# Performance work log

Hardware: AMD Instinct MI355X
Metric: run time of the kernel (lower is better)

The kernel has to match this reference:

```python
import jax, jax.numpy as jnp
import numpy as np
import math

B, C, H, W, K, HID = 8, 64, 512, 512, 8, 64

def setup_inputs() -> dict:
    key = jax.random.key(0)
    ks = jax.random.split(key, 12)
    s = 0.05  # weight scale
    return {
        "x": jax.random.normal(ks[0], (B, C, H, W), dtype=jnp.float32),
        "w1k": jax.random.normal(ks[1], (1, HID), dtype=jnp.float32) * s,
        "b1k": jax.random.normal(ks[2], (HID,), dtype=jnp.float32) * s,
        "w2k": jax.random.normal(ks[3], (HID, K * K), dtype=jnp.float32) * s,
        "b2k": jax.random.normal(ks[4], (K * K,), dtype=jnp.float32) * s,
        "w1b": jax.random.normal(ks[5], (1, HID), dtype=jnp.float32) * s,
        "b1b": jax.random.normal(ks[6], (HID,), dtype=jnp.float32) * s,
        "w2b": jax.random.normal(ks[7], (HID, 1), dtype=jnp.float32) * s,
        "b2b": jax.random.normal(ks[8], (1,), dtype=jnp.float32) * s,
        "conv_w": jax.random.normal(ks[9], (C, C), dtype=jnp.float32) * s,
        "conv_b": jax.random.normal(ks[10], (C,), dtype=jnp.float32) * s,
    }

def _patch_pos_dist(h, w, k):
    # normalized distance of each KxK patch center from the image center, row-major over (nh, nw)
    nh, nw = h // k, w // k
    cy, cx = h / 2.0, w / 2.0
    max_d = math.sqrt(cy ** 2 + cx ** 2)
    py = jnp.arange(nh, dtype=jnp.float32) * k + k / 2.0
    px = jnp.arange(nw, dtype=jnp.float32) * k + k / 2.0
    d = jnp.sqrt((py - cy)[:, None] ** 2 + (px - cx)[None, :] ** 2) / max_d
    return d.reshape(nh * nw)  # [L]

def reference(x, w1k, b1k, w2k, b2k, w1b, b1b, w2b, b2b, conv_w, conv_b):
    b, c, h, w = x.shape
    kk = w2k.shape[1]
    k = int(round(math.sqrt(kk)))
    nh, nw = h // k, w // k
    L = nh * nw

    d = _patch_pos_dist(h, w, k)[:, None]  # [L, 1]
    # dynamic per-patch-position kernels and bias (exact-erf GELU as in torch default)
    pk = jax.nn.gelu(d @ w1k + b1k, approximate=False) @ w2k + b2k          # [L, K*K]
    pb = (jax.nn.gelu(d @ w1b + b1b, approximate=False) @ w2b + b2b)[:, 0]  # [L]

    # non-overlapping unfold: [B, C, K*K, L], patches row-major over (nh, nw)
    patches = (x.reshape(b, c, nh, k, nw, k)
                 .transpose(0, 1, 2, 4, 3, 5)
                 .reshape(b, c, L, kk)
                 .transpose(0, 1, 3, 2))

    feats = jnp.einsum('bckl,lk->bcl', patches, pk) + pb[None, None, :]     # [B, C, L]
    feats = jnp.einsum('oc,bcl->bol', conv_w, feats) + conv_b[None, :, None]  # 1x1 conv

    mod = patches * feats[:, :, None, :]  # [B, C, K*K, L]

    # fold back (non-overlapping, so a pure reshape/scatter)
    out = (mod.transpose(0, 1, 3, 2)
              .reshape(b, c, nh, nw, k, k)
              .transpose(0, 1, 2, 4, 3, 5)
              .reshape(b, c, h, w))
    return out
```

## Files before the change

### kernel.cpp

```cpp
#include <hip/hip_runtime.h>
#include <math.h>


static __device__ __forceinline__ float gelu_erf(float x) {
    return 0.5f * x * (1.0f + erff(x * 0.70710678118654752f));
}

__global__ __launch_bounds__(256) void mlp_precompute(
    const float* __restrict__ w1k, const float* __restrict__ b1k,
    const float* __restrict__ w2k, const float* __restrict__ b2k,
    const float* __restrict__ w1b, const float* __restrict__ b1b,
    const float* __restrict__ w2b, const float* __restrict__ b2b,
    float* __restrict__ pk_out,
    float* __restrict__ pb_out)
{
    constexpr int HID = 64;
    const int tid = threadIdx.x;
    const int pi  = tid >> 6;
    const int j   = tid & 63;
    const int l   = blockIdx.x * 4 + pi;

    const int py_i = l >> 6;
    const int px_i = l & 63;
    const float py = (float)(py_i * 8) + 4.0f - 256.0f;
    const float px = (float)(px_i * 8) + 4.0f - 256.0f;
    const float dd = sqrtf(py * py + px * px) * (1.0f / 362.03867196751236f);

    __shared__ float gk[4][HID];
    __shared__ float gb[4][HID];

    gk[pi][j] = gelu_erf(dd * w1k[j] + b1k[j]);
    gb[pi][j] = gelu_erf(dd * w1b[j] + b1b[j]);
    __syncthreads();

    float s = b2k[j];
#pragma unroll 8
    for (int h = 0; h < HID; ++h)
        s += gk[pi][h] * w2k[h * HID + j];
    pk_out[l * HID + j] = s;

    if (j == 0) {
        float t = b2b[0];
        for (int h = 0; h < HID; ++h)
            t += gb[pi][h] * w2b[h];
        pb_out[l] = t;
    }
}

__global__ __launch_bounds__(512) void afpm_main(
    const float* __restrict__ x,
    const float* __restrict__ conv_w, const float* __restrict__ conv_b,
    const float* __restrict__ pk_g,
    const float* __restrict__ pb_g,
    float* __restrict__ out)
{
    constexpr int C   = 64;
    constexpr int H   = 512;
    constexpr int W   = 512;
    constexpr int PWG = 4;

    const int tid = threadIdx.x;
    const int q   = tid & 1;
    const int pw  = (tid >> 1) & 3;
    const int c   = tid >> 3;
    const int pwg = blockIdx.x;
    const int ph  = blockIdx.y;
    const int b   = blockIdx.z;

    const int pw_glob = pwg * PWG + pw;

    __shared__ float pkL[PWG][64];
    __shared__ float pbL[PWG];
    __shared__ float f0L[C][PWG];
    __shared__ float ftL[C][PWG];

    const size_t base = (((size_t)b * C + c) * H + (size_t)ph * 8) * W
                        + (size_t)pw_glob * 8 + (size_t)q * 4;
    const float* xp = x + base;
    float4 v[8];
#pragma unroll
    for (int r = 0; r < 8; ++r)
        v[r] = *(const float4*)(xp + (size_t)r * W);

    const int lbase = ph * 64 + pwg * 4;
    if (tid < 256)
        pkL[tid >> 6][tid & 63] = pk_g[((size_t)lbase + (tid >> 6)) * 64 + (tid & 63)];
    else if (tid < 256 + PWG)
        pbL[tid - 256] = pb_g[lbase + (tid - 256)];
    __syncthreads();

    float s = 0.0f;
#pragma unroll
    for (int r = 0; r < 8; ++r) {
        const float4 a = v[r];
        const int k0 = r * 8 + q * 4;
        s += a.x * pkL[pw][k0 + 0] + a.y * pkL[pw][k0 + 1]
           + a.z * pkL[pw][k0 + 2] + a.w * pkL[pw][k0 + 3];
    }
    s += __shfl_xor(s, 1);
    if (q == 0)
        f0L[c][pw] = s + pbL[pw];
    __syncthreads();

    if (tid < 256) {
        const int o   = tid >> 2;
        const int pw2 = tid & 3;
        float t = conv_b[o];
#pragma unroll 8
        for (int cc = 0; cc < C; ++cc)
            t += conv_w[o * C + cc] * f0L[cc][pw2];
        ftL[o][pw2] = t;
    }
    __syncthreads();

    const float m = ftL[c][pw];
    float* op = out + base;
#pragma unroll
    for (int r = 0; r < 8; ++r) {
        float4 a = v[r];
        a.x *= m; a.y *= m; a.z *= m; a.w *= m;
        *(float4*)(op + (size_t)r * W) = a;
    }
}

extern "C" void kernel_launch(void* const* d_in, const int* in_sizes, int n_in,
                              void* d_out, int out_size, void* d_ws, size_t ws_size,
                              hipStream_t stream) {
    const float* x      = (const float*)d_in[0];
    const float* w1k    = (const float*)d_in[1];
    const float* b1k    = (const float*)d_in[2];
    const float* w2k    = (const float*)d_in[3];
    const float* b2k    = (const float*)d_in[4];
    const float* w1b    = (const float*)d_in[5];
    const float* b1b    = (const float*)d_in[6];
    const float* w2b    = (const float*)d_in[7];
    const float* b2b    = (const float*)d_in[8];
    const float* conv_w = (const float*)d_in[9];
    const float* conv_b = (const float*)d_in[10];
    float* out = (float*)d_out;

    constexpr int L = 64 * 64;
    float* pk = (float*)d_ws;
    float* pb = pk + (size_t)L * 64;

    mlp_precompute<<<L / 4, 256, 0, stream>>>(w1k, b1k, w2k, b2k,
                                              w1b, b1b, w2b, b2b, pk, pb);

    dim3 grid(16, 64, 8);
    afpm_main<<<grid, 512, 0, stream>>>(x, conv_w, conv_b, pk, pb, out);
}
```

Baseline: 240.8 us.

## Make blocks loop over a patch row with register double-buffered loads

Each block now covers a whole row of patches for one batch. It loops over 16 groups of four patches and prefetches the next group's rows into a second register buffer while computing the current one. conv_w is transposed into shared memory once per block, and the patch bias is folded in through precomputed conv weight row sums. The aim is to amortise the per-block setup and hide load latency, at the cost of fewer blocks, higher register pressure and a barrier per step.

```diff
diff --git a/kernel.cpp b/kernel.cpp
--- a/kernel.cpp
+++ b/kernel.cpp
@@ -47,80 +47,114 @@
     }
 }
 
-__global__ __launch_bounds__(512) void afpm_main(
+__global__ __launch_bounds__(512, 4) void afpm_main(
     const float* __restrict__ x,
     const float* __restrict__ conv_w, const float* __restrict__ conv_b,
     const float* __restrict__ pk_g,
     const float* __restrict__ pb_g,
     float* __restrict__ out)
 {
-    constexpr int C   = 64;
-    constexpr int H   = 512;
     constexpr int W   = 512;
-    constexpr int PWG = 4;
+    constexpr int PKS = 68;
 
     const int tid = threadIdx.x;
     const int q   = tid & 1;
     const int pw  = (tid >> 1) & 3;
     const int c   = tid >> 3;
-    const int pwg = blockIdx.x;
-    const int ph  = blockIdx.y;
-    const int b   = blockIdx.z;
+    const int b   = blockIdx.x >> 6;
+    const int ph  = blockIdx.x & 63;
 
-    const int pw_glob = pwg * PWG + pw;
+    __shared__ float convT[64 * 64];
+    __shared__ __align__(16) float pkAll[64 * PKS];
+    __shared__ float pbAll[64];
+    __shared__ float rowsumL[64];
+    __shared__ float f0L[2][64][4];
 
-    __shared__ float pkL[PWG][64];
-    __shared__ float pbL[PWG];
-    __shared__ float f0L[C][PWG];
-    __shared__ float ftL[C][PWG];
+    const size_t cbase = (((size_t)b * 64 + c) * 512 + (size_t)ph * 8) * (size_t)W
+                         + (size_t)(pw * 8 + q * 4);
 
-    const size_t base = (((size_t)b * C + c) * H + (size_t)ph * 8) * W
-                        + (size_t)pw_glob * 8 + (size_t)q * 4;
-    const float* xp = x + base;
-    float4 v[8];
+    float4 vA[8], vB[8];
+    {
+        const float* xp = x + cbase;
 #pragma unroll
-    for (int r = 0; r < 8; ++r)
-        v[r] = *(const float4*)(xp + (size_t)r * W);
+        for (int r = 0; r < 8; ++r)
+            vA[r] = *(const float4*)(xp + r * W);
+    }
 
-    const int lbase = ph * 64 + pwg * 4;
-    if (tid < 256)
-        pkL[tid >> 6][tid & 63] = pk_g[((size_t)lbase + (tid >> 6)) * 64 + (tid & 63)];
-    else if (tid < 256 + PWG)
-        pbL[tid - 256] = pb_g[lbase + (tid - 256)];
-    __syncthreads();
+    {
+        const float4* cw4 = (const float4*)conv_w;
+        const float4  w0  = cw4[tid * 2 + 0];
+        const float4  w1  = cw4[tid * 2 + 1];
+        const int o   = tid >> 3;
+        const int cc0 = (tid & 7) * 8;
+        convT[(cc0 + 0) * 64 + o] = w0.x; convT[(cc0 + 1) * 64 + o] = w0.y;
+        convT[(cc0 + 2) * 64 + o] = w0.z; convT[(cc0 + 3) * 64 + o] = w0.w;
+        convT[(cc0 + 4) * 64 + o] = w1.x; convT[(cc0 + 5) * 64 + o] = w1.y;
+        convT[(cc0 + 6) * 64 + o] = w1.z; convT[(cc0 + 7) * 64 + o] = w1.w;
 
-    float s = 0.0f;
-#pragma unroll
-    for (int r = 0; r < 8; ++r) {
-        const float4 a = v[r];
-        const int k0 = r * 8 + q * 4;
-        s += a.x * pkL[pw][k0 + 0] + a.y * pkL[pw][k0 + 1]
-           + a.z * pkL[pw][k0 + 2] + a.w * pkL[pw][k0 + 3];
-    }
-    s += __shfl_xor(s, 1);
-    if (q == 0)
-        f0L[c][pw] = s + pbL[pw];
-    __syncthreads();
+        const float4* pk4 = (const float4*)(pk_g + (size_t)(ph * 64) * 64);
+        const float4  k0  = pk4[tid * 2 + 0];
+        const float4  k1  = pk4[tid * 2 + 1];
+        const int l  = tid >> 3;
+        const int kk = (tid & 7) * 8;
+        *(float4*)&pkAll[l * PKS + kk + 0] = k0;
+        *(float4*)&pkAll[l * PKS + kk + 4] = k1;
 
-    if (tid < 256) {
-        const int o   = tid >> 2;
-        const int pw2 = tid & 3;
-        float t = conv_b[o];
-#pragma unroll 8
-        for (int cc = 0; cc < C; ++cc)
-            t += conv_w[o * C + cc] * f0L[cc][pw2];
-        ftL[o][pw2] = t;
+        if (tid < 64) pbAll[tid] = pb_g[ph * 64 + tid];
     }
     __syncthreads();
 
-    const float m = ftL[c][pw];
-    float* op = out + base;
-#pragma unroll
-    for (int r = 0; r < 8; ++r) {
-        float4 a = v[r];
-        a.x *= m; a.y *= m; a.z *= m; a.w *= m;
-        *(float4*)(op + (size_t)r * W) = a;
+    if (tid < 64) {
+        float s = 0.0f;
+#pragma unroll 8
+        for (int cc = 0; cc < 64; ++cc) s += convT[cc * 64 + tid];
+        rowsumL[tid] = s;
     }
+
+    const float cb = conv_b[c];
+
+#define STEP(G, VC, VN, PRE, PAR)                                           \
+    {                                                                       \
+        if (PRE) {                                                          \
+            const float* xn = x + cbase + ((G) + 1) * 32;                   \
+            _Pragma("unroll")                                               \
+            for (int r = 0; r < 8; ++r)                                     \
+                VN[r] = *(const float4*)(xn + r * W);                       \
+        }                                                                   \
+        const int l = (G) * 4 + pw;                                         \
+        const float* pkp = &pkAll[l * PKS + q * 4];                         \
+        float s = 0.0f;                                                     \
+        _Pragma("unroll")                                                   \
+        for (int r = 0; r < 8; ++r) {                                       \
+            const float4 a  = VC[r];                                        \
+            const float4 kv = *(const float4*)(pkp + r * 8);                \
+            s += a.x * kv.x + a.y * kv.y + a.z * kv.z + a.w * kv.w;         \
+        }                                                                   \
+        s += __shfl_xor(s, 1);                                              \
+        if (q == 0) f0L[PAR][c][pw] = s;                                    \
+        __syncthreads();                                                    \
+        float t = 0.0f;                                                     \
+        _Pragma("unroll 8")                                                 \
+        for (int i = 0; i < 32; ++i) {                                      \
+            const int cc = q * 32 + i;                                      \
+            t += convT[cc * 64 + c] * f0L[PAR][cc][pw];                     \
+        }                                                                   \
+        t += __shfl_xor(t, 1);                                              \
+        const float m = t + cb + pbAll[l] * rowsumL[c];                     \
+        float* op = out + cbase + (G) * 32;                                 \
+        _Pragma("unroll")                                                   \
+        for (int r = 0; r < 8; ++r) {                                       \
+            float4 a = VC[r];                                               \
+            a.x *= m; a.y *= m; a.z *= m; a.w *= m;                         \
+            *(float4*)(op + r * W) = a;                                     \
+        }                                                                   \
+    }
+
+    for (int g = 0; g < 16; g += 2) {
+        STEP(g,     vA, vB, true,            0);
+        STEP(g + 1, vB, vA, ((g + 1) < 15),  1);
+    }
+#undef STEP
 }
 
 extern "C" void kernel_launch(void* const* d_in, const int* in_sizes, int n_in,
@@ -146,6 +180,5 @@
     mlp_precompute<<<L / 4, 256, 0, stream>>>(w1k, b1k, w2k, b2k,
                                               w1b, b1b, w2b, b2b, pk, pb);
 
-    dim3 grid(16, 64, 8);
-    afpm_main<<<grid, 512, 0, stream>>>(x, conv_w, conv_b, pk, pb, out);
+    afpm_main<<<512, 512, 0, stream>>>(x, conv_w, conv_b, pk, pb, out);
 }
```

New measurement: 262.9 us. 9.2% more time.
